# Optimization experiments

Measured on AMD Instinct MI355X. Metric: run time of the kernel, lower is better.

## Reference

```python
import jax, jax.numpy as jnp
import numpy as np

B, S, H = 2, 1024, 4096
NQ, NKV, D = 32, 8, 128
I = 11008
EPS = 1e-5


def _rope_tables(seq_len, head_dim, base=10000.0):
    inv_freq = 1.0 / (base ** (np.arange(0, head_dim, 2, dtype=np.float32) / head_dim))
    t = np.arange(seq_len, dtype=np.float32)
    freqs = np.outer(t, inv_freq)                      # [S, D/2]
    emb = np.concatenate([freqs, freqs], axis=-1)      # [S, D]
    return jnp.asarray(np.cos(emb)), jnp.asarray(np.sin(emb))


def setup_inputs() -> dict:
    key = jax.random.key(0)
    ks = jax.random.split(key, 9)
    sc = 0.02
    cos, sin = _rope_tables(S, D)
    return {
        "x": jax.random.normal(ks[0], (B, S, H), jnp.float32),
        "cos": cos,
        "sin": sin,
        "attn_norm_w": jnp.ones((H,), jnp.float32),
        "ffn_norm_w": jnp.ones((H,), jnp.float32),
        "wq": jax.random.normal(ks[1], (H, NQ * D), jnp.float32) * sc,
        "wk": jax.random.normal(ks[2], (H, NKV * D), jnp.float32) * sc,
        "wv": jax.random.normal(ks[3], (H, NKV * D), jnp.float32) * sc,
        "wo": jax.random.normal(ks[4], (NQ * D, H), jnp.float32) * sc,
        "w_gate": jax.random.normal(ks[5], (H, I), jnp.float32) * sc,
        "w_up": jax.random.normal(ks[6], (H, I), jnp.float32) * sc,
        "w_down": jax.random.normal(ks[7], (I, H), jnp.float32) * sc,
    }


def _rmsnorm(x, w, eps=EPS):
    var = jnp.mean(jnp.square(x), axis=-1, keepdims=True)
    return x * jax.lax.rsqrt(var + eps) * w


def _rotate_half(x):
    x1, x2 = jnp.split(x, 2, axis=-1)
    return jnp.concatenate([-x2, x1], axis=-1)


def _apply_rope(q, k, cos, sin):
    # q: [B,S,NQ,D], k: [B,S,NKV,D]; cos/sin: [S,D] -> broadcast [1,S,1,D]
    c = cos[None, :, None, :]
    s = sin[None, :, None, :]
    return q * c + _rotate_half(q) * s, k * c + _rotate_half(k) * s


def reference(x, cos, sin, attn_norm_w, ffn_norm_w, wq, wk, wv, wo, w_gate, w_up, w_down):
    # ---- attention block (pre-norm, context/prefill path, causal) ----
    h_in = _rmsnorm(x, attn_norm_w)
    q = (h_in @ wq).reshape(B, S, NQ, D)
    k = (h_in @ wk).reshape(B, S, NKV, D)
    v = (h_in @ wv).reshape(B, S, NKV, D)
    q, k = _apply_rope(q, k, cos, sin)

    n_rep = NQ // NKV
    k = jnp.repeat(k, n_rep, axis=2)  # [B,S,NQ,D]
    v = jnp.repeat(v, n_rep, axis=2)

    scale = 1.0 / jnp.sqrt(jnp.float32(D))
    scores = jnp.einsum("bqhd,bkhd->bhqk", q, k) * scale  # [B,NQ,S,S]
    causal = jnp.tril(jnp.ones((S, S), bool))
    scores = jnp.where(causal[None, None], scores, -jnp.inf)
    probs = jax.nn.softmax(scores, axis=-1)
    attn = jnp.einsum("bhqk,bkhd->bqhd", probs, v).reshape(B, S, NQ * D)
    h = x + attn @ wo

    # ---- MLP block (pre-norm SwiGLU) ----
    m_in = _rmsnorm(h, ffn_norm_w)
    mlp = (jax.nn.silu(m_in @ w_gate) * (m_in @ w_up)) @ w_down
    return h + mlp
```

## Files before the change

### kernel.cpp

```cpp
#include <hip/hip_runtime.h>
#include <cstdint>
#include <cstddef>


typedef __bf16 bf16;
typedef __attribute__((ext_vector_type(8))) __bf16 bf16x8;
typedef __attribute__((ext_vector_type(4))) float f32x4;

#define GLDS16(gptr, lptr)                                                    \
  __builtin_amdgcn_global_load_lds(                                           \
      (const __attribute__((address_space(1))) void*)(gptr),                  \
      (__attribute__((address_space(3))) void*)(lptr), 16, 0, 0)

#define S_LEN 1024
#define H_DIM 4096
#define NQ_H 32
#define NKV_H 8
#define HD 128
#define I_DIM 11008

__global__ __launch_bounds__(256) void wtrans64_kernel(
    const float* __restrict__ src, bf16* __restrict__ dst, int K, int N,
    int tile_stride, int base) {
  const int tid = threadIdx.x;
  const int n0 = blockIdx.x * 64, k0 = blockIdx.y * 64;
  __shared__ float t[64][65];
  const int r = tid >> 4, c4 = (tid & 15) * 4;
#pragma unroll
  for (int j = 0; j < 4; j++) {
    const float4 v =
        *(const float4*)&src[(size_t)(k0 + r + j * 16) * N + n0 + c4];
    t[r + j * 16][c4 + 0] = v.x;
    t[r + j * 16][c4 + 1] = v.y;
    t[r + j * 16][c4 + 2] = v.z;
    t[r + j * 16][c4 + 3] = v.w;
  }
  __syncthreads();
  const int n = tid >> 2, kq = (tid & 3) * 16;
  bf16x8 o0, o1;
#pragma unroll
  for (int i = 0; i < 8; i++) {
    o0[i] = (bf16)t[kq + i][n];
    o1[i] = (bf16)t[kq + 8 + i][n];
  }
  const int ng = n0 + n;
  const size_t orow = (size_t)(ng >> 7) * tile_stride + (ng & 127) + base;
  *(bf16x8*)&dst[orow * K + k0 + kq] = o0;
  *(bf16x8*)&dst[orow * K + k0 + kq + 8] = o1;
}

__global__ __launch_bounds__(256) void rmsnorm_kernel(
    const float* __restrict__ x, const float* __restrict__ w,
    bf16* __restrict__ out) {
  const int row = blockIdx.x;
  const float4* xr = (const float4*)(x + (size_t)row * H_DIM);
  float4 v[4];
  float s = 0.f;
#pragma unroll
  for (int i = 0; i < 4; i++) {
    v[i] = xr[threadIdx.x + i * 256];
    s += v[i].x * v[i].x + v[i].y * v[i].y + v[i].z * v[i].z + v[i].w * v[i].w;
  }
#pragma unroll
  for (int m = 1; m < 64; m <<= 1) s += __shfl_xor(s, m);
  __shared__ float red[4];
  if ((threadIdx.x & 63) == 0) red[threadIdx.x >> 6] = s;
  __syncthreads();
  s = red[0] + red[1] + red[2] + red[3];
  const float r = rsqrtf(s * (1.f / H_DIM) + 1e-5f);
  bf16* o = out + (size_t)row * H_DIM;
  const float4* wr = (const float4*)w;
#pragma unroll
  for (int i = 0; i < 4; i++) {
    float4 wv = wr[threadIdx.x + i * 256];
    int idx = (threadIdx.x + i * 256) * 4;
    o[idx + 0] = (bf16)(v[i].x * r * wv.x);
    o[idx + 1] = (bf16)(v[i].y * r * wv.y);
    o[idx + 2] = (bf16)(v[i].z * r * wv.z);
    o[idx + 3] = (bf16)(v[i].w * r * wv.w);
  }
}

template <int MODE>
__global__ __launch_bounds__(256) void gemm_tn(
    const bf16* __restrict__ A, const bf16* __restrict__ Bt,
    void* __restrict__ Cout, const float* __restrict__ resid,
    int N, int K) {
  __shared__ __align__(16) bf16 As[128 * 32];
  __shared__ __align__(16) bf16 Bs[128 * 32];
  const int tid = threadIdx.x;
  const int wave = tid >> 6, lane = tid & 63;
  const int lr = lane & 15, quad = lane >> 4;
  const int m0 = (blockIdx.x & 15) * 128, n0 = (blockIdx.x >> 4) * 128;
  const int wm = (wave & 1) * 64, wn = (wave >> 1) * 64;

  const int c0 = wave * 2;
  const int ar0 = (c0 * 64 + lane) >> 2;
  const int ar1 = (c0 * 64 + 64 + lane) >> 2;
  const int acol = (lane & 3) * 8;
  const bf16* Ag0 = A + (size_t)(m0 + ar0) * K + acol;
  const bf16* Ag1 = A + (size_t)(m0 + ar1) * K + acol;
  const bf16* Bg0 = Bt + (size_t)(n0 + ar0) * K + acol;
  const bf16* Bg1 = Bt + (size_t)(n0 + ar1) * K + acol;
  bf16* As0 = As + c0 * 512;
  bf16* Bs0 = Bs + c0 * 512;

  f32x4 acc[4][4] = {};

  for (int k0 = 0; k0 < K; k0 += 32) {
    __syncthreads();
    GLDS16(Ag0 + k0, As0);
    GLDS16(Ag1 + k0, As0 + 512);
    GLDS16(Bg0 + k0, Bs0);
    GLDS16(Bg1 + k0, Bs0 + 512);
    __syncthreads();
    bf16x8 af[4], bfr[4];
#pragma unroll
    for (int i = 0; i < 4; i++)
      af[i] = *(const bf16x8*)&As[(wm + i * 16 + lr) * 32 + quad * 8];
#pragma unroll
    for (int j = 0; j < 4; j++)
      bfr[j] = *(const bf16x8*)&Bs[(wn + j * 16 + lr) * 32 + quad * 8];
#pragma unroll
    for (int i = 0; i < 4; i++)
#pragma unroll
      for (int j = 0; j < 4; j++)
        acc[i][j] = __builtin_amdgcn_mfma_f32_16x16x32_bf16(af[i], bfr[j],
                                                            acc[i][j], 0, 0, 0);
  }

#pragma unroll
  for (int i = 0; i < 4; i++)
#pragma unroll
    for (int j = 0; j < 4; j++)
#pragma unroll
      for (int r = 0; r < 4; r++) {
        const size_t row = m0 + wm + i * 16 + quad * 4 + r;
        const size_t col = n0 + wn + j * 16 + lr;
        const float v = acc[i][j][r];
        if (MODE == 0)
          ((bf16*)Cout)[row * N + col] = (bf16)v;
        else if (MODE == 1)
          ((float*)Cout)[row * N + col] = v;
        else
          ((float*)Cout)[row * N + col] = v + resid[row * N + col];
      }
}

__global__ __launch_bounds__(256) void rope_kernel(
    const bf16* __restrict__ qkv, const float* __restrict__ cosT,
    const float* __restrict__ sinT, bf16* __restrict__ qb,
    bf16* __restrict__ kb) {
  const int row = blockIdx.x;
  const int s = row & (S_LEN - 1);
  const bf16* base = qkv + (size_t)row * 6144;
  const float scale = 0.08838834764831845f;
  for (int p = threadIdx.x; p < 2560; p += 256) {
    const int hd = p >> 6;
    const int d = p & 63;
    const float c = cosT[s * HD + d], sn = sinT[s * HD + d];
    if (hd < NQ_H) {
      const bf16* qp = base + hd * HD;
      const float x1 = (float)qp[d], x2 = (float)qp[d + 64];
      bf16* o = qb + (size_t)row * H_DIM + hd * HD;
      o[d] = (bf16)((x1 * c - x2 * sn) * scale);
      o[d + 64] = (bf16)((x2 * c + x1 * sn) * scale);
    } else {
      const int kh = hd - NQ_H;
      const bf16* kp = base + H_DIM + kh * HD;
      const float x1 = (float)kp[d], x2 = (float)kp[d + 64];
      bf16* o = kb + (size_t)row * (NKV_H * HD) + kh * HD;
      o[d] = (bf16)(x1 * c - x2 * sn);
      o[d + 64] = (bf16)(x2 * c + x1 * sn);
    }
  }
}

__global__ __launch_bounds__(256) void vtrans_kernel(
    const bf16* __restrict__ qkv, bf16* __restrict__ vt) {
  const int tx = threadIdx.x & 31, ty = threadIdx.x >> 5;
  const int s0 = blockIdx.x * 32, d0 = blockIdx.y * 32;
  const int b = blockIdx.z >> 3, kv = blockIdx.z & 7;
  __shared__ float t[32][33];
#pragma unroll
  for (int j = 0; j < 4; j++) {
    const int s = s0 + ty + j * 8;
    t[ty + j * 8][tx] =
        (float)qkv[(size_t)(b * S_LEN + s) * 6144 + 5120 + kv * HD + d0 + tx];
  }
  __syncthreads();
#pragma unroll
  for (int j = 0; j < 4; j++) {
    const int d = d0 + ty + j * 8;
    vt[((size_t)(b * NKV_H + kv) * HD + d) * S_LEN + s0 + tx] =
        (bf16)t[tx][ty + j * 8];
  }
}

__global__ __launch_bounds__(256) void attn_fwd(
    const bf16* __restrict__ Qb, const bf16* __restrict__ Kb,
    const bf16* __restrict__ Vtb, bf16* __restrict__ Ob) {
  __shared__ __align__(16) bf16 Ks[16 * 512];
  __shared__ __align__(16) bf16 Vs[16 * 512];
  __shared__ __align__(16) bf16 Ps[16 * 512];
  const int tid = threadIdx.x;
  const int wave = tid >> 6, lane = tid & 63;
  const int lr = lane & 15, quad = lane >> 4;
  const int qt = blockIdx.x, h = blockIdx.y, b = blockIdx.z;
  const int kv = h >> 2;
  const int qrow0 = qt * 128 + wave * 32;

  bf16x8 qf[2][4];
#pragma unroll
  for (int mi = 0; mi < 2; mi++)
#pragma unroll
    for (int ks = 0; ks < 4; ks++)
      qf[mi][ks] = *(const bf16x8*)&Qb[(size_t)(b * S_LEN + qrow0 + mi * 16 + lr) *
                                           H_DIM +
                                       h * HD + ks * 32 + quad * 8];

  f32x4 oacc[2][8] = {};
  float m_i[2][4], l_i[2][4];
#pragma unroll
  for (int mi = 0; mi < 2; mi++)
#pragma unroll
    for (int r = 0; r < 4; r++) {
      m_i[mi][r] = -__builtin_inff();
      l_i[mi][r] = 0.f;
    }

  const int nk = 2 * (qt + 1);
  const int maxrow = qrow0 + 31;
  const int srow = lane >> 2;
  const int scol = (lane & 3) * 8;

  for (int kt = 0; kt < nk; kt++) {
    const int k0 = kt * 64;
    __syncthreads();
#pragma unroll
    for (int i = 0; i < 4; i++) {
      const int c = wave * 4 + i;
      {
        const int ks = c >> 2, sc = c & 3;
        const int key = sc * 16 + srow;
        GLDS16(Kb + (size_t)(b * S_LEN + k0 + key) * (NKV_H * HD) + kv * HD +
                   ks * 32 + scol,
               Ks + c * 512);
      }
      {
        const int ks2 = c >> 3, sc2 = c & 7;
        const int d = sc2 * 16 + srow;
        GLDS16(Vtb + ((size_t)(b * NKV_H + kv) * HD + d) * S_LEN + k0 +
                   ks2 * 32 + scol,
               Vs + c * 512);
      }
    }
    __syncthreads();
    const bool active = (k0 <= maxrow);
    float alpha[2][4];
    if (active) {
      f32x4 sacc[2][4];
#pragma unroll
      for (int mi = 0; mi < 2; mi++)
#pragma unroll
        for (int nj = 0; nj < 4; nj++) sacc[mi][nj] = (f32x4){0.f, 0.f, 0.f, 0.f};
#pragma unroll
      for (int ks = 0; ks < 4; ks++) {
        bf16x8 kf[4];
#pragma unroll
        for (int nj = 0; nj < 4; nj++)
          kf[nj] = *(const bf16x8*)&Ks[ks * 2048 + (nj * 16 + lr) * 32 + quad * 8];
#pragma unroll
        for (int mi = 0; mi < 2; mi++)
#pragma unroll
          for (int nj = 0; nj < 4; nj++)
            sacc[mi][nj] = __builtin_amdgcn_mfma_f32_16x16x32_bf16(
                qf[mi][ks], kf[nj], sacc[mi][nj], 0, 0, 0);
      }
#pragma unroll
      for (int mi = 0; mi < 2; mi++) {
#pragma unroll
        for (int r = 0; r < 4; r++) {
          const int row = qrow0 + mi * 16 + quad * 4 + r;
          float best = -__builtin_inff();
#pragma unroll
          for (int nj = 0; nj < 4; nj++) {
            const int col = k0 + nj * 16 + lr;
            if (col > row) sacc[mi][nj][r] = -__builtin_inff();
            best = fmaxf(best, sacc[mi][nj][r]);
          }
#pragma unroll
          for (int m = 1; m < 16; m <<= 1)
            best = fmaxf(best, __shfl_xor(best, m));
          const float mnew = fmaxf(m_i[mi][r], best);
          alpha[mi][r] = __expf(m_i[mi][r] - mnew);
          m_i[mi][r] = mnew;
          float ssum = 0.f;
#pragma unroll
          for (int nj = 0; nj < 4; nj++) {
            const float p = __expf(sacc[mi][nj][r] - mnew);
            sacc[mi][nj][r] = p;
            ssum += p;
          }
#pragma unroll
          for (int m = 1; m < 16; m <<= 1) ssum += __shfl_xor(ssum, m);
          l_i[mi][r] = l_i[mi][r] * alpha[mi][r] + ssum;
        }
      }
#pragma unroll
      for (int mi = 0; mi < 2; mi++)
#pragma unroll
        for (int dj = 0; dj < 8; dj++)
#pragma unroll
          for (int r = 0; r < 4; r++) oacc[mi][dj][r] *= alpha[mi][r];
#pragma unroll
      for (int mi = 0; mi < 2; mi++)
#pragma unroll
        for (int nj = 0; nj < 4; nj++) {
          const int ks2 = nj >> 1;
          const int k32 = (nj & 1) * 16 + lr;
#pragma unroll
          for (int r = 0; r < 4; r++) {
            const int rowl = wave * 32 + mi * 16 + quad * 4 + r;
            Ps[ks2 * 4096 + rowl * 32 + k32] = (bf16)sacc[mi][nj][r];
          }
        }
    }
    __syncthreads();
    if (active) {
#pragma unroll
      for (int ks2 = 0; ks2 < 2; ks2++) {
        bf16x8 pf[2], vf[8];
#pragma unroll
        for (int mi = 0; mi < 2; mi++)
          pf[mi] = *(const bf16x8*)&Ps[ks2 * 4096 +
                                       (wave * 32 + mi * 16 + lr) * 32 + quad * 8];
#pragma unroll
        for (int dj = 0; dj < 8; dj++)
          vf[dj] = *(const bf16x8*)&Vs[ks2 * 4096 + (dj * 16 + lr) * 32 + quad * 8];
#pragma unroll
        for (int mi = 0; mi < 2; mi++)
#pragma unroll
          for (int dj = 0; dj < 8; dj++)
            oacc[mi][dj] = __builtin_amdgcn_mfma_f32_16x16x32_bf16(
                pf[mi], vf[dj], oacc[mi][dj], 0, 0, 0);
      }
    }
  }
#pragma unroll
  for (int mi = 0; mi < 2; mi++)
#pragma unroll
    for (int r = 0; r < 4; r++) {
      const float rinv = 1.f / l_i[mi][r];
      const size_t row = (size_t)b * S_LEN + qrow0 + mi * 16 + quad * 4 + r;
#pragma unroll
      for (int dj = 0; dj < 8; dj++)
        Ob[row * H_DIM + h * HD + dj * 16 + lr] =
            (bf16)(oacc[mi][dj][r] * rinv);
    }
}

__global__ __launch_bounds__(256) void swiglu_kernel(
    const bf16* __restrict__ gu, bf16* __restrict__ act) {
  const int gid = blockIdx.x * 256 + threadIdx.x;
  const int row = gid / 1376;
  const int c8 = (gid % 1376) * 8;
  const size_t gbase = (size_t)row * 22016 + (size_t)(c8 >> 7) * 256 + (c8 & 127);
  bf16x8 g = *(const bf16x8*)&gu[gbase];
  bf16x8 u = *(const bf16x8*)&gu[gbase + 128];
  bf16x8 o;
#pragma unroll
  for (int j = 0; j < 8; j++) {
    const float gf = (float)g[j];
    const float sg = gf / (1.f + __expf(-gf));
    o[j] = (bf16)(sg * (float)u[j]);
  }
  *(bf16x8*)&act[(size_t)row * I_DIM + c8] = o;
}

extern "C" void kernel_launch(void* const* d_in, const int* in_sizes, int n_in,
                              void* d_out, int out_size, void* d_ws,
                              size_t ws_size, hipStream_t stream) {
  const float* x = (const float*)d_in[0];
  const float* cosT = (const float*)d_in[1];
  const float* sinT = (const float*)d_in[2];
  const float* anw = (const float*)d_in[3];
  const float* fnw = (const float*)d_in[4];
  const float* wq = (const float*)d_in[5];
  const float* wk = (const float*)d_in[6];
  const float* wv = (const float*)d_in[7];
  const float* wo = (const float*)d_in[8];
  const float* wg = (const float*)d_in[9];
  const float* wu = (const float*)d_in[10];
  const float* wd = (const float*)d_in[11];

  char* ws = (char*)d_ws;
  size_t off = 0;
  auto alloc = [&](size_t bytes) -> void* {
    void* p = ws + off;
    off += (bytes + 255) & ~(size_t)255;
    return p;
  };
  const size_t M = 2048;
  bf16* WGUt = (bf16*)alloc(22016ULL * 4096 * 2);
  bf16* WDt = (bf16*)alloc(4096ULL * I_DIM * 2);
  char* R1 = (char*)alloc(90177536);
  char* bufY = (char*)alloc(83886080);
  float* H2 = (float*)alloc(M * 4096 * 4);
  bf16* MINb = (bf16*)alloc(M * 4096 * 2);

  bf16* WQKVt = (bf16*)R1;
  bf16* WOt = (bf16*)(R1 + 50331648);
  bf16* GU = (bf16*)R1;
  bf16* HIN = (bf16*)bufY;
  bf16* QKVb = HIN + M * 4096;
  bf16* QB = QKVb + M * 6144;
  bf16* KB = QB + M * 4096;
  bf16* VT = KB + M * 1024;
  bf16* ATTN = VT + M * 1024;
  bf16* ACT = (bf16*)bufY;

  wtrans64_kernel<<<dim3(64, 64), 256, 0, stream>>>(wq, WQKVt, 4096, 4096, 128, 0);
  wtrans64_kernel<<<dim3(16, 64), 256, 0, stream>>>(wk, WQKVt + 4096ULL * 4096, 4096, 1024, 128, 0);
  wtrans64_kernel<<<dim3(16, 64), 256, 0, stream>>>(wv, WQKVt + 5120ULL * 4096, 4096, 1024, 128, 0);
  wtrans64_kernel<<<dim3(64, 64), 256, 0, stream>>>(wo, WOt, 4096, 4096, 128, 0);
  wtrans64_kernel<<<dim3(172, 64), 256, 0, stream>>>(wg, WGUt, 4096, I_DIM, 256, 0);
  wtrans64_kernel<<<dim3(172, 64), 256, 0, stream>>>(wu, WGUt, 4096, I_DIM, 256, 128);
  wtrans64_kernel<<<dim3(64, 172), 256, 0, stream>>>(wd, WDt, I_DIM, 4096, 128, 0);

  rmsnorm_kernel<<<2048, 256, 0, stream>>>(x, anw, HIN);
  gemm_tn<0><<<48 * 16, 256, 0, stream>>>(HIN, WQKVt, QKVb, nullptr, 6144, 4096);
  rope_kernel<<<2048, 256, 0, stream>>>(QKVb, cosT, sinT, QB, KB);
  vtrans_kernel<<<dim3(32, 4, 16), 256, 0, stream>>>(QKVb, VT);
  attn_fwd<<<dim3(8, 32, 2), 256, 0, stream>>>(QB, KB, VT, ATTN);
  gemm_tn<2><<<32 * 16, 256, 0, stream>>>(ATTN, WOt, H2, x, 4096, 4096);
  rmsnorm_kernel<<<2048, 256, 0, stream>>>(H2, fnw, MINb);
  gemm_tn<0><<<172 * 16, 256, 0, stream>>>(MINb, WGUt, GU, nullptr, 22016, 4096);
  swiglu_kernel<<<11008, 256, 0, stream>>>(GU, ACT);
  gemm_tn<2><<<32 * 16, 256, 0, stream>>>(ACT, WDt, d_out, H2, 4096, I_DIM);
}
```

Measured before the change: 1.886 ms.

## Replace GEMM with 256-wide tiled double-buffered, swizzled LDS pipelined kernel

Replaces the simple 128x128, K=32 single-buffered GEMM with a 512-thread kernel using BMx256 tiles, K=64 steps, double-buffered LDS with XOR swizzling, and async global->LDS loads interleaved with MFMA phases under barriers and setprio. It aims to hide memory latency, cut LDS bank conflicts and raise operand reuse per tile. All four projection GEMMs switch to it, with larger M tiles for the QKV and gate/up GEMMs. The cost is more complex hand-scheduled synchronization and fewer blocks, which can leave CUs underused on the smaller N=4096 GEMMs.

```diff
diff --git a/kernel.cpp b/kernel.cpp
--- a/kernel.cpp
+++ b/kernel.cpp
@@ -81,67 +81,199 @@
   }
 }
 
-template <int MODE>
-__global__ __launch_bounds__(256) void gemm_tn(
+template <int BM, int MODE>
+__global__ __launch_bounds__(512, 2) void gemm256(
     const bf16* __restrict__ A, const bf16* __restrict__ Bt,
-    void* __restrict__ Cout, const float* __restrict__ resid,
-    int N, int K) {
-  __shared__ __align__(16) bf16 As[128 * 32];
-  __shared__ __align__(16) bf16 Bs[128 * 32];
+    void* __restrict__ Cout, const float* __restrict__ resid, int N, int K,
+    int mshift) {
+  constexpr int MREP = BM / 32;
+  constexpr int MQ = MREP / 2;
+  constexpr int LA = BM / 128;
+  constexpr int ABYTES = BM * 128;
+  constexpr int BUFB = ABYTES + 32768;
+  __shared__ __align__(16) char smem[2 * BUFB];
+
   const int tid = threadIdx.x;
-  const int wave = tid >> 6, lane = tid & 63;
+  const int w = tid >> 6, lane = tid & 63;
   const int lr = lane & 15, quad = lane >> 4;
-  const int m0 = (blockIdx.x & 15) * 128, n0 = (blockIdx.x >> 4) * 128;
-  const int wm = (wave & 1) * 64, wn = (wave >> 1) * 64;
-
-  const int c0 = wave * 2;
-  const int ar0 = (c0 * 64 + lane) >> 2;
-  const int ar1 = (c0 * 64 + 64 + lane) >> 2;
-  const int acol = (lane & 3) * 8;
-  const bf16* Ag0 = A + (size_t)(m0 + ar0) * K + acol;
-  const bf16* Ag1 = A + (size_t)(m0 + ar1) * K + acol;
-  const bf16* Bg0 = Bt + (size_t)(n0 + ar0) * K + acol;
-  const bf16* Bg1 = Bt + (size_t)(n0 + ar1) * K + acol;
-  bf16* As0 = As + c0 * 512;
-  bf16* Bs0 = Bs + c0 * 512;
-
-  f32x4 acc[4][4] = {};
-
-  for (int k0 = 0; k0 < K; k0 += 32) {
-    __syncthreads();
-    GLDS16(Ag0 + k0, As0);
-    GLDS16(Ag1 + k0, As0 + 512);
-    GLDS16(Bg0 + k0, Bs0);
-    GLDS16(Bg1 + k0, Bs0 + 512);
-    __syncthreads();
-    bf16x8 af[4], bfr[4];
-#pragma unroll
-    for (int i = 0; i < 4; i++)
-      af[i] = *(const bf16x8*)&As[(wm + i * 16 + lr) * 32 + quad * 8];
-#pragma unroll
-    for (int j = 0; j < 4; j++)
-      bfr[j] = *(const bf16x8*)&Bs[(wn + j * 16 + lr) * 32 + quad * 8];
-#pragma unroll
-    for (int i = 0; i < 4; i++)
-#pragma unroll
-      for (int j = 0; j < 4; j++)
-        acc[i][j] = __builtin_amdgcn_mfma_f32_16x16x32_bf16(af[i], bfr[j],
-                                                            acc[i][j], 0, 0, 0);
-  }
-
-#pragma unroll
-  for (int i = 0; i < 4; i++)
-#pragma unroll
-    for (int j = 0; j < 4; j++)
+  const int wm = w & 1, wn = w >> 1;
+  const int m0 = (blockIdx.x & ((1 << mshift) - 1)) * BM;
+  const int n0 = (blockIdx.x >> mshift) * 256;
+  const int NT = K >> 6;
+
+  const int lrow = lane >> 3;
+  const int lcbe = ((lane & 7) ^ lrow) << 3;
+  const bf16* aS[2][LA];
+#pragma unroll
+  for (int h = 0; h < 2; h++)
+#pragma unroll
+    for (int j = 0; j < LA; j++)
+      aS[h][j] =
+          A + (size_t)(m0 + h * (BM / 2) + j * 64 + w * 8 + lrow) * K + lcbe;
+  const bf16* bS[2][2];
+#pragma unroll
+  for (int h = 0; h < 2; h++)
+#pragma unroll
+    for (int j = 0; j < 2; j++)
+      bS[h][j] =
+          Bt + (size_t)(n0 + h * 128 + j * 64 + w * 8 + lrow) * K + lcbe;
+  const int sdst = w * 1024;
+
+#pragma unroll
+  for (int h = 0; h < 2; h++)
+#pragma unroll
+    for (int j = 0; j < 2; j++)
+      GLDS16(bS[h][j], smem + ABYTES + h * 16384 + j * 8192 + sdst);
+#pragma unroll
+  for (int h = 0; h < 2; h++)
+#pragma unroll
+    for (int j = 0; j < LA; j++)
+      GLDS16(aS[h][j], smem + h * (BM * 64) + j * 8192 + sdst);
+#pragma unroll
+  for (int h = 0; h < 2; h++)
+#pragma unroll
+    for (int j = 0; j < 2; j++)
+      GLDS16(bS[h][j] + 64, smem + BUFB + ABYTES + h * 16384 + j * 8192 + sdst);
+  asm volatile("s_waitcnt vmcnt(4)" ::: "memory");
+  __builtin_amdgcn_s_barrier();
+
+  const int swz = (lr & 7) << 4;
+  const int abase = (wm * (BM / 2) + lr) * 128;
+  const int bbase = ABYTES + (wn * 64 + lr) * 128;
+  const int pcb0 = (quad * 16) ^ swz;
+
+  f32x4 acc[MREP][4] = {};
+  bf16x8 af[MQ][2], bfr[2][2][2];
+
+  for (int t = 0; t < NT; ++t) {
+    char* cb_ = smem + (t & 1) * BUFB;
+    char* nb_ = smem + ((t & 1) ^ 1) * BUFB;
+
+#pragma unroll
+    for (int i4 = 0; i4 < MQ; i4++)
+#pragma unroll
+      for (int kk = 0; kk < 2; kk++)
+        af[i4][kk] = *(const bf16x8*)(cb_ + abase + i4 * (16 * 128) +
+                                      (pcb0 ^ (kk * 64)));
+#pragma unroll
+    for (int j2 = 0; j2 < 2; j2++)
+#pragma unroll
+      for (int kk = 0; kk < 2; kk++)
+        bfr[0][j2][kk] = *(const bf16x8*)(cb_ + bbase + j2 * (16 * 128) +
+                                          (pcb0 ^ (kk * 64)));
+    if (t + 1 < NT) {
+#pragma unroll
+      for (int j = 0; j < LA; j++)
+        GLDS16(aS[0][j] + (size_t)(t + 1) * 64, nb_ + j * 8192 + sdst);
+    }
+    __builtin_amdgcn_s_barrier();
+    asm volatile("s_waitcnt lgkmcnt(0)" ::: "memory");
+    __builtin_amdgcn_sched_barrier(0);
+    __builtin_amdgcn_s_setprio(1);
+#pragma unroll
+    for (int i4 = 0; i4 < MQ; i4++)
+#pragma unroll
+      for (int j2 = 0; j2 < 2; j2++)
+#pragma unroll
+        for (int kk = 0; kk < 2; kk++)
+          acc[i4][j2] = __builtin_amdgcn_mfma_f32_16x16x32_bf16(
+              af[i4][kk], bfr[0][j2][kk], acc[i4][j2], 0, 0, 0);
+    __builtin_amdgcn_s_setprio(0);
+    __builtin_amdgcn_s_barrier();
+
+#pragma unroll
+    for (int j2 = 0; j2 < 2; j2++)
+#pragma unroll
+      for (int kk = 0; kk < 2; kk++)
+        bfr[1][j2][kk] =
+            *(const bf16x8*)(cb_ + bbase + (32 + j2 * 16) * 128 +
+                             (pcb0 ^ (kk * 64)));
+    if (t + 1 < NT) {
+#pragma unroll
+      for (int j = 0; j < LA; j++)
+        GLDS16(aS[1][j] + (size_t)(t + 1) * 64,
+               nb_ + BM * 64 + j * 8192 + sdst);
+    }
+    __builtin_amdgcn_s_barrier();
+    asm volatile("s_waitcnt lgkmcnt(0)" ::: "memory");
+    __builtin_amdgcn_sched_barrier(0);
+    __builtin_amdgcn_s_setprio(1);
+#pragma unroll
+    for (int i4 = 0; i4 < MQ; i4++)
+#pragma unroll
+      for (int j2 = 0; j2 < 2; j2++)
+#pragma unroll
+        for (int kk = 0; kk < 2; kk++)
+          acc[i4][2 + j2] = __builtin_amdgcn_mfma_f32_16x16x32_bf16(
+              af[i4][kk], bfr[1][j2][kk], acc[i4][2 + j2], 0, 0, 0);
+    __builtin_amdgcn_s_setprio(0);
+    __builtin_amdgcn_s_barrier();
+
+#pragma unroll
+    for (int i4 = 0; i4 < MQ; i4++)
+#pragma unroll
+      for (int kk = 0; kk < 2; kk++)
+        af[i4][kk] =
+            *(const bf16x8*)(cb_ + abase + ((BM / 4) + i4 * 16) * 128 +
+                             (pcb0 ^ (kk * 64)));
+    if (t + 2 < NT) {
+#pragma unroll
+      for (int j = 0; j < 2; j++)
+        GLDS16(bS[0][j] + (size_t)(t + 2) * 64,
+               cb_ + ABYTES + j * 8192 + sdst);
+    }
+    __builtin_amdgcn_s_barrier();
+    asm volatile("s_waitcnt lgkmcnt(0)" ::: "memory");
+    __builtin_amdgcn_sched_barrier(0);
+    __builtin_amdgcn_s_setprio(1);
+#pragma unroll
+    for (int i4 = 0; i4 < MQ; i4++)
+#pragma unroll
+      for (int j2 = 0; j2 < 2; j2++)
+#pragma unroll
+        for (int kk = 0; kk < 2; kk++)
+          acc[MQ + i4][j2] = __builtin_amdgcn_mfma_f32_16x16x32_bf16(
+              af[i4][kk], bfr[0][j2][kk], acc[MQ + i4][j2], 0, 0, 0);
+    __builtin_amdgcn_s_setprio(0);
+    __builtin_amdgcn_s_barrier();
+
+    if (t + 2 < NT) {
+#pragma unroll
+      for (int j = 0; j < 2; j++)
+        GLDS16(bS[1][j] + (size_t)(t + 2) * 64,
+               cb_ + ABYTES + 16384 + j * 8192 + sdst);
+    }
+    __builtin_amdgcn_s_barrier();
+    asm volatile("s_waitcnt lgkmcnt(0)" ::: "memory");
+    __builtin_amdgcn_sched_barrier(0);
+    __builtin_amdgcn_s_setprio(1);
+#pragma unroll
+    for (int i4 = 0; i4 < MQ; i4++)
+#pragma unroll
+      for (int j2 = 0; j2 < 2; j2++)
+#pragma unroll
+        for (int kk = 0; kk < 2; kk++)
+          acc[MQ + i4][2 + j2] = __builtin_amdgcn_mfma_f32_16x16x32_bf16(
+              af[i4][kk], bfr[1][j2][kk], acc[MQ + i4][2 + j2], 0, 0, 0);
+    __builtin_amdgcn_s_setprio(0);
+    if (t + 2 < NT)
+      asm volatile("s_waitcnt vmcnt(4)" ::: "memory");
+    else
+      asm volatile("s_waitcnt vmcnt(0)" ::: "memory");
+    __builtin_amdgcn_s_barrier();
+  }
+
+#pragma unroll
+  for (int ai = 0; ai < MREP; ai++)
+#pragma unroll
+    for (int bj = 0; bj < 4; bj++)
 #pragma unroll
       for (int r = 0; r < 4; r++) {
-        const size_t row = m0 + wm + i * 16 + quad * 4 + r;
-        const size_t col = n0 + wn + j * 16 + lr;
-        const float v = acc[i][j][r];
+        const size_t row = m0 + wm * (BM / 2) + ai * 16 + quad * 4 + r;
+        const size_t col = n0 + wn * 64 + bj * 16 + lr;
+        const float v = acc[ai][bj][r];
         if (MODE == 0)
           ((bf16*)Cout)[row * N + col] = (bf16)v;
-        else if (MODE == 1)
-          ((float*)Cout)[row * N + col] = v;
         else
           ((float*)Cout)[row * N + col] = v + resid[row * N + col];
       }
@@ -429,13 +561,13 @@
   wtrans64_kernel<<<dim3(64, 172), 256, 0, stream>>>(wd, WDt, I_DIM, 4096, 128, 0);
 
   rmsnorm_kernel<<<2048, 256, 0, stream>>>(x, anw, HIN);
-  gemm_tn<0><<<48 * 16, 256, 0, stream>>>(HIN, WQKVt, QKVb, nullptr, 6144, 4096);
+  gemm256<256, 0><<<8 * 24, 512, 0, stream>>>(HIN, WQKVt, QKVb, nullptr, 6144, 4096, 3);
   rope_kernel<<<2048, 256, 0, stream>>>(QKVb, cosT, sinT, QB, KB);
   vtrans_kernel<<<dim3(32, 4, 16), 256, 0, stream>>>(QKVb, VT);
   attn_fwd<<<dim3(8, 32, 2), 256, 0, stream>>>(QB, KB, VT, ATTN);
-  gemm_tn<2><<<32 * 16, 256, 0, stream>>>(ATTN, WOt, H2, x, 4096, 4096);
+  gemm256<128, 2><<<16 * 16, 512, 0, stream>>>(ATTN, WOt, H2, x, 4096, 4096, 4);
   rmsnorm_kernel<<<2048, 256, 0, stream>>>(H2, fnw, MINb);
-  gemm_tn<0><<<172 * 16, 256, 0, stream>>>(MINb, WGUt, GU, nullptr, 22016, 4096);
+  gemm256<256, 0><<<8 * 86, 512, 0, stream>>>(MINb, WGUt, GU, nullptr, 22016, 4096, 3);
   swiglu_kernel<<<11008, 256, 0, stream>>>(GU, ACT);
-  gemm_tn<2><<<32 * 16, 256, 0, stream>>>(ACT, WDt, d_out, H2, 4096, I_DIM);
-}
+  gemm256<128, 2><<<16 * 16, 512, 0, stream>>>(ACT, WDt, d_out, H2, 4096, 11008, 4);
+}
```

New measurement: 1.546 ms. 18.0% less time.
